# Performance work log

Hardware: AMD Instinct MI355X
Metric: run time of the kernel (lower is better)

Reference implementation:

```python
import jax, jax.numpy as jnp
import numpy as np

SUBSTEPS = 8  # fixed substeps per save interval (replaces diffrax adaptive PID control)

# Tsit5 (Tsitouras 2011) Butcher tableau, 5th-order solution weights
C2, C3, C4, C5, C6 = 0.161, 0.327, 0.9, 0.9800255409045097, 1.0
A21 = 0.161
A31, A32 = -0.008480655492356989, 0.335480655492357
A41, A42, A43 = 2.8971530571054935, -6.359448489975075, 4.3622954328695815
A51, A52, A53, A54 = 5.325864828439257, -11.748883564062828, 7.4955393428898365, -0.09249506636175525
A61, A62, A63, A64, A65 = 5.86145544294642, -12.92096931784711, 8.159367898576159, -0.071584973281401, -0.028269050394068383
B1, B2, B3, B4, B5, B6 = 0.09646076681806523, 0.01, 0.4798896504144996, 1.379008574103742, -3.290069515436081, 2.324710524099774

# SEIAR epidemiological constants (hardcoded in NODE.RHS)
KK, AA, II, P, F, EE, DD, Q = 0.526, 0.244, 0.244, 0.667, 0.98, 0.0, 1.0, 0.5


def setup_inputs() -> dict:
    key = jax.random.key(0)
    ks = jax.random.split(key, 4)
    W = 64  # width_size

    def lin(k, out_d, in_d):
        lim = 1.0 / np.sqrt(in_d)
        kw, kb = jax.random.split(k)
        w = jax.random.uniform(kw, (out_d, in_d), minval=-lim, maxval=lim, dtype=jnp.float32)
        b = jax.random.uniform(kb, (out_d,), minval=-lim, maxval=lim, dtype=jnp.float32)
        return w, b

    w_in, b_in = lin(ks[0], W, 1)   # MLP: 1 -> W
    w_h, b_h = lin(ks[1], W, W)     # W -> W (depth=2 => one hidden-to-hidden layer)
    w_out, b_out = lin(ks[2], 1, W) # W -> 1

    return {
        "y0_ignored": jax.random.normal(ks[3], (5,), dtype=jnp.float32),
        "ts": jnp.arange(1024, dtype=jnp.float32),
        "state_vec": jnp.array([5.0, -5.0, 0.0, -5.0, -5.0], dtype=jnp.float32),
        "w_in": w_in, "b_in": b_in,
        "w_h": w_h, "b_h": b_h,
        "w_out": w_out, "b_out": b_out,
        "scales": jnp.ones((5,), dtype=jnp.float32),
    }


def reference(y0_ignored, ts, state_vec, w_in, b_in, w_h, b_h, w_out, b_out, scales):
    def beta(t):
        h = jax.nn.softplus(w_in @ jnp.atleast_1d(t) + b_in)
        h = jax.nn.softplus(w_h @ h + b_h)
        o = w_out @ h + b_out
        return jax.nn.sigmoid(1e-4 * o)[0]

    def rhs(t, y):
        S, E, I, A, R = y * scales
        b = beta(t)
        LL = EE * E + (1.0 - Q) * I + DD * A
        dS = -b * S * LL
        dE = b * S * LL - KK * E
        dI = P * KK * E - AA * I
        dA = (1.0 - P) * KK * E - II * A
        dR = F * AA * I + II * A
        return jnp.stack([dS, dE, dI, dA, dR]) / scales

    def tsit5_step(t, y, h):
        k1 = rhs(t, y)
        k2 = rhs(t + C2 * h, y + h * A21 * k1)
        k3 = rhs(t + C3 * h, y + h * (A31 * k1 + A32 * k2))
        k4 = rhs(t + C4 * h, y + h * (A41 * k1 + A42 * k2 + A43 * k3))
        k5 = rhs(t + C5 * h, y + h * (A51 * k1 + A52 * k2 + A53 * k3 + A54 * k4))
        k6 = rhs(t + C6 * h, y + h * (A61 * k1 + A62 * k2 + A63 * k3 + A64 * k4 + A65 * k5))
        return y + h * (B1 * k1 + B2 * k2 + B3 * k3 + B4 * k4 + B5 * k5 + B6 * k6)

    y0 = jax.nn.softmax(state_vec) / scales  # learned initial condition, normalized

    def interval(y, tt):
        t0, t1 = tt
        h = (t1 - t0) / SUBSTEPS
        def body(yc, i):
            return tsit5_step(t0 + i.astype(yc.dtype) * h, yc, h), None
        y, _ = jax.lax.scan(body, y, jnp.arange(SUBSTEPS))
        return y, y

    _, ys = jax.lax.scan(interval, y0, (ts[:-1], ts[1:]))  # [T-1, 5]
    states_norm = jnp.concatenate([y0[None], ys], axis=0)  # [T, 5]
    return states_norm * scales
```

## Files before the change

kernel.cpp:

```cpp
#include <hip/hip_runtime.h>
#include <math.h>


#define NCHUNK 32
#define NTOTAL 1280
#define NPROD  (NTOTAL - NCHUNK)
#define TS     64
#define BURN_MAX_POLLS 16384

#define NI 1032
#define NH 1028
#define NI_ALLOC 1048
#define NH_ALLOC 1040
#define NCT 66

#define A21f 0.161f
#define A31f -0.008480655492356989f
#define A32f 0.335480655492357f
#define A41f 2.8971530571054935f
#define A42f -6.359448489975075f
#define A43f 4.3622954328695815f
#define A51f 5.325864828439257f
#define A52f -11.748883564062828f
#define A53f 7.4955393428898365f
#define A54f -0.09249506636175525f
#define A61f 5.86145544294642f
#define A62f -12.92096931784711f
#define A63f 8.159367898576159f
#define A64f -0.071584973281401f
#define A65f -0.028269050394068383f
#define B1f 0.09646076681806523f
#define B2f 0.01f
#define B3f 0.4798896504144996f
#define B4f 1.379008574103742f
#define B5f -3.290069515436081f
#define B6f 2.324710524099774f

typedef float v2f __attribute__((ext_vector_type(2)));
__device__ __forceinline__ v2f vfma(v2f a, v2f b, v2f c) {
    return __builtin_elementwise_fma(a, b, c);
}
__device__ __forceinline__ v2f splat2(float x) { return (v2f){x, x}; }

struct Bounds { int s[NCHUNK + 1]; };

__device__ const float g_cstage[6] = {
    0.0f, 0.161f, 0.327f, 0.9f, 0.9800255409045097f, 1.0f};

__device__ __forceinline__ float softplus_f(float x) {
    return fmaxf(x, 0.0f) + log1pf(expf(-fabsf(x)));
}
__device__ __forceinline__ int imin(int a, int b) { return a < b ? a : b; }

#define cKK  0.526f
#define cAA  0.244f
#define cII  0.244f
#define cPKK ((float)(0.667 * 0.526))
#define cQKK ((float)((1.0 - 0.667) * 0.526))
#define cFAA ((float)(0.98 * 0.244))

__device__ __forceinline__ void rhs2(v2f zSE, v2f zIA, float b,
                                     v2f& kSE, v2f& kIA, float& kR) {
    float S = zSE.x, E = zSE.y, I = zIA.x, A = zIA.y;
    float LL = fmaf(0.5f, I, A);
    float T  = (b * S) * LL;
    kSE = (v2f){-T, fmaf(-cKK, E, T)};
    kIA = (v2f){fmaf(cPKK, E, -cAA * I), fmaf(cQKK, E, -cII * A)};
    kR  = fmaf(cFAA, I, cII * A);
}

struct Tab2 {
    v2f a21,a31,a32,a41,a42,a43,a51,a52,a53,a54;
    v2f a61,a62,a63,a64,a65,b1,b2,b3,b4,b5,b6;
};
__device__ __forceinline__ Tab2 make_tab2(float h) {
    Tab2 t;
    t.a21=splat2(A21f*h); t.a31=splat2(A31f*h); t.a32=splat2(A32f*h);
    t.a41=splat2(A41f*h); t.a42=splat2(A42f*h); t.a43=splat2(A43f*h);
    t.a51=splat2(A51f*h); t.a52=splat2(A52f*h); t.a53=splat2(A53f*h);
    t.a54=splat2(A54f*h); t.a61=splat2(A61f*h); t.a62=splat2(A62f*h);
    t.a63=splat2(A63f*h); t.a64=splat2(A64f*h); t.a65=splat2(A65f*h);
    t.b1=splat2(B1f*h); t.b2=splat2(B2f*h); t.b3=splat2(B3f*h);
    t.b4=splat2(B4f*h); t.b5=splat2(B5f*h); t.b6=splat2(B6f*h);
    return t;
}

#define FOLD(dSE,dIA,dR, c, kSE,kIA,kR, pSE,pIA,pR) \
    dSE = vfma(T.c, kSE, pSE); dIA = vfma(T.c, kIA, pIA); \
    dR  = fmaf(T.c.x, kR, pR);

__device__ __forceinline__ void t5_step(v2f& zSE, v2f& zIA, float& zR,
                                        const Tab2& T, const float bc[6]) {
    v2f k1SE,k1IA,k2SE,k2IA,k3SE,k3IA,k4SE,k4IA,k5SE,k5IA,k6SE,k6IA;
    float k1R,k2R,k3R,k4R,k5R,k6R;
    v2f tSE,tIA,pSE,pIA; float tR,pR;

    rhs2(zSE,zIA,bc[0],k1SE,k1IA,k1R);
    FOLD(tSE,tIA,tR, a21, k1SE,k1IA,k1R, zSE,zIA,zR);
    rhs2(tSE,tIA,bc[1],k2SE,k2IA,k2R);
    FOLD(pSE,pIA,pR, a31, k1SE,k1IA,k1R, zSE,zIA,zR);
    FOLD(tSE,tIA,tR, a32, k2SE,k2IA,k2R, pSE,pIA,pR);
    rhs2(tSE,tIA,bc[2],k3SE,k3IA,k3R);
    FOLD(pSE,pIA,pR, a41, k1SE,k1IA,k1R, zSE,zIA,zR);
    FOLD(pSE,pIA,pR, a42, k2SE,k2IA,k2R, pSE,pIA,pR);
    FOLD(tSE,tIA,tR, a43, k3SE,k3IA,k3R, pSE,pIA,pR);
    rhs2(tSE,tIA,bc[3],k4SE,k4IA,k4R);
    FOLD(pSE,pIA,pR, a51, k1SE,k1IA,k1R, zSE,zIA,zR);
    FOLD(pSE,pIA,pR, a52, k2SE,k2IA,k2R, pSE,pIA,pR);
    FOLD(pSE,pIA,pR, a53, k3SE,k3IA,k3R, pSE,pIA,pR);
    FOLD(tSE,tIA,tR, a54, k4SE,k4IA,k4R, pSE,pIA,pR);
    rhs2(tSE,tIA,bc[4],k5SE,k5IA,k5R);
    FOLD(pSE,pIA,pR, a61, k1SE,k1IA,k1R, zSE,zIA,zR);
    FOLD(pSE,pIA,pR, a62, k2SE,k2IA,k2R, pSE,pIA,pR);
    FOLD(pSE,pIA,pR, a63, k3SE,k3IA,k3R, pSE,pIA,pR);
    FOLD(pSE,pIA,pR, a64, k4SE,k4IA,k4R, pSE,pIA,pR);
    FOLD(tSE,tIA,tR, a65, k5SE,k5IA,k5R, pSE,pIA,pR);
    rhs2(tSE,tIA,bc[5],k6SE,k6IA,k6R);
    FOLD(pSE,pIA,pR, b1, k1SE,k1IA,k1R, zSE,zIA,zR);
    FOLD(pSE,pIA,pR, b2, k2SE,k2IA,k2R, pSE,pIA,pR);
    FOLD(pSE,pIA,pR, b3, k3SE,k3IA,k3R, pSE,pIA,pR);
    FOLD(pSE,pIA,pR, b4, k4SE,k4IA,k4R, pSE,pIA,pR);
    FOLD(pSE,pIA,pR, b5, k5SE,k5IA,k5R, pSE,pIA,pR);
    FOLD(zSE,zIA,zR, b6, k6SE,k6IA,k6R, pSE,pIA,pR);
}

__device__ __forceinline__ void rk4_step(v2f& zSE, v2f& zIA, float& zR,
                                         v2f h2v, v2f hv, v2f h6v,
                                         float b0, float bm, float b1) {
    v2f k1SE,k1IA,k2SE,k2IA,k3SE,k3IA,k4SE,k4IA;
    float k1R,k2R,k3R,k4R;
    v2f tSE,tIA; float tR;
    const v2f two = splat2(2.0f);

    rhs2(zSE,zIA,b0,k1SE,k1IA,k1R);
    tSE=vfma(h2v,k1SE,zSE); tIA=vfma(h2v,k1IA,zIA); tR=fmaf(h2v.x,k1R,zR);
    rhs2(tSE,tIA,bm,k2SE,k2IA,k2R);
    tSE=vfma(h2v,k2SE,zSE); tIA=vfma(h2v,k2IA,zIA); tR=fmaf(h2v.x,k2R,zR);
    rhs2(tSE,tIA,bm,k3SE,k3IA,k3R);
    tSE=vfma(hv,k3SE,zSE);  tIA=vfma(hv,k3IA,zIA);  tR=fmaf(hv.x,k3R,zR);
    v2f PSE = vfma(two, k2SE + k3SE, k1SE);
    v2f PIA = vfma(two, k2IA + k3IA, k1IA);
    float PR = fmaf(2.0f, k2R + k3R, k1R);
    rhs2(tSE,tIA,b1,k4SE,k4IA,k4R);
    zSE = vfma(h6v, PSE + k4SE, zSE);
    zIA = vfma(h6v, PIA + k4IA, zIA);
    zR  = fmaf(h6v.x, PR + k4R, zR);
}

__device__ __forceinline__ float aload(const float* p) {
    return __hip_atomic_load(p, __ATOMIC_RELAXED, __HIP_MEMORY_SCOPE_AGENT);
}
__device__ __forceinline__ bool ok3(const float v[3]) {
    return (v[0] > 0.0f) && (v[1] > 0.0f) && (v[2] > 0.0f);
}
__device__ __forceinline__ bool ok6(const float v[6]) {
    return (v[0]>0.f)&&(v[1]>0.f)&&(v[2]>0.f)&&(v[3]>0.f)&&(v[4]>0.f)&&(v[5]>0.f);
}
__device__ __forceinline__ void loadF(float v[3], const float* bi,
                                      const float* bh, int i) {
    v[0] = aload(bi + i); v[1] = aload(bh + i); v[2] = aload(bi + i + 1);
}
__device__ __forceinline__ void loadC(float v[3], const float* bi, int j) {
    const float* p = bi + 256 + 4 * j;
    v[0] = aload(p); v[1] = aload(p + 2); v[2] = aload(p + 4);
}
__device__ __forceinline__ void load6(float v[6], const float* p) {
#pragma unroll
    for (int j = 0; j < 6; ++j) v[j] = aload(p + j);
}

__global__ __launch_bounds__(64, 1) void fused_kernel(
    const float* __restrict__ ts,
    const float* __restrict__ state_vec,
    const float* __restrict__ w_in, const float* __restrict__ b_in,
    const float* __restrict__ w_h,  const float* __restrict__ b_h,
    const float* __restrict__ w_out, const float* __restrict__ b_out,
    float* __restrict__ beta_int, float* __restrict__ beta_half,
    float* __restrict__ beta_cT,
    float* __restrict__ done_arr, float* __restrict__ out,
    Bounds B)
{
    int b    = blockIdx.x;
    int lane = threadIdx.x;

    if (b >= NCHUNK) {
        int p = b - NCHUNK;
        const int TtlPair = 2 * NH;
        const int Ttl = NCT * 6 + TtlPair + (NI - NH);
        float t0g = ts[0], hf = ts[1] - ts[0];
        float wi = w_in[lane], bi_ = b_in[lane];
        float bhh = b_h[lane], wo = w_out[lane];
        float bo = b_out[0];
        const float* __restrict__ wr = w_h + (lane << 6);

        for (int e = p; e < Ttl; e += NPROD) {
            float t; float* dst;
            if (e < NCT * 6) {
                int row = e / 6, st = e - row * 6;
                t = t0g + (4.0f * row + 4.0f * g_cstage[st]) * hf;
                dst = beta_cT + row * 8 + st;
            } else if (e < NCT * 6 + TtlPair) {
                int idx = e - NCT * 6;
                int i = idx >> 1;
                if (idx & 1) { t = t0g + ((float)i + 0.5f) * hf; dst = beta_half + i; }
                else         { t = t0g + (float)i * hf;          dst = beta_int + i;  }
            } else {
                int i = NH + (e - NCT * 6 - TtlPair);
                t = t0g + (float)i * hf; dst = beta_int + i;
            }
            float h1 = softplus_f(fmaf(wi, t, bi_));
            float acc = bhh;
#pragma unroll
            for (int k = 0; k < 64; ++k)
                acc = fmaf(wr[k], __shfl(h1, k, 64), acc);
            float h2 = softplus_f(acc);
            float pr = wo * h2;
#pragma unroll
            for (int off = 32; off > 0; off >>= 1)
                pr += __shfl_down(pr, off, 64);
            if (lane == 0) {
                float o  = pr + bo;
                float bb = 1.0f / (1.0f + expf(-1e-4f * o));
                __hip_atomic_store(dst, bb, __ATOMIC_RELAXED,
                                   __HIP_MEMORY_SCOPE_AGENT);
            }
        }

        float x[8];
#pragma unroll
        for (int j = 0; j < 8; ++j) x[j] = 1.0f + (float)(lane + j) * 1e-12f;
        for (int outer = 0; outer < BURN_MAX_POLLS; ++outer) {
            for (int i2 = 0; i2 < 40; ++i2) {
#pragma unroll
                for (int j = 0; j < 8; ++j)
                    x[j] = fmaf(x[j], 0.99999988f, 1e-9f);
            }
            float f = aload(done_arr + (lane & 31));
            if (__all(f == 1.0f)) break;
        }
        float r = 0.0f;
#pragma unroll
        for (int j = 0; j < 8; ++j) r += x[j];
        if (r == 123456.0f) done_arr[63] = r;
        return;
    }

    if (lane != 0) return;

    int start = B.s[b];
    int end   = B.s[b + 1];
    int nf    = end - start;
    float hf  = ts[1] - ts[0];

    v2f zSE, zIA; float zR;
    {
        float v[5], zz[5];
#pragma unroll
        for (int s = 0; s < 5; ++s) v[s] = state_vec[s];
        float m = v[0];
#pragma unroll
        for (int s = 1; s < 5; ++s) m = fmaxf(m, v[s]);
        float sum = 0.0f;
#pragma unroll
        for (int s = 0; s < 5; ++s) { zz[s] = expf(v[s] - m); sum += zz[s]; }
        float inv = 1.0f / sum;
#pragma unroll
        for (int s = 0; s < 5; ++s) zz[s] *= inv;
        zSE = (v2f){zz[0], zz[1]}; zIA = (v2f){zz[2], zz[3]}; zR = zz[4];
        if (b == 0) {
#pragma unroll
            for (int s = 0; s < 5; ++s) out[s] = zz[s];
        }
    }

    if (nf > 0) {
        int nc = start / 4;
        int nT = imin(nc, TS);
        int nR = nc - nT;

        if (nT > 0) {
            Tab2 T = make_tab2(4.0f * hf);
            float r0[6], r1[6], bc[6];
            load6(r0, beta_cT);
            load6(r1, beta_cT + 8);
            int i = 0;
            for (; i + 2 <= nT; i += 2) {
                const float* p0 = beta_cT + i * 8;
                while (!ok6(r0)) load6(r0, p0);
#pragma unroll
                for (int j = 0; j < 6; ++j) bc[j] = r0[j];
                load6(r0, p0 + 16);
                t5_step(zSE, zIA, zR, T, bc);
                const float* p1 = p0 + 8;
                while (!ok6(r1)) load6(r1, p1);
#pragma unroll
                for (int j = 0; j < 6; ++j) bc[j] = r1[j];
                load6(r1, p1 + 16);
                t5_step(zSE, zIA, zR, T, bc);
            }
            if (i < nT) {
                const float* p0 = beta_cT + i * 8;
                while (!ok6(r0)) load6(r0, p0);
#pragma unroll
                for (int j = 0; j < 6; ++j) bc[j] = r0[j];
                t5_step(zSE, zIA, zR, T, bc);
            }
        }

        if (nR > 0) {
            v2f h2v = splat2(2.0f * hf), hv = splat2(4.0f * hf),
                h6v = splat2(4.0f * hf / 6.0f);
            float r0[3], r1[3], r2[3], r3[3];
            loadC(r0, beta_int, 0); loadC(r1, beta_int, 1);
            loadC(r2, beta_int, 2); loadC(r3, beta_int, 3);
            int j = 0;
#define CSTEP(R, jj) { \
            while (!ok3(R)) loadC(R, beta_int, (jj)); \
            float b0_=R[0], bm_=R[1], b1_=R[2]; \
            loadC(R, beta_int, (jj) + 4); \
            rk4_step(zSE, zIA, zR, h2v, hv, h6v, b0_, bm_, b1_); }
            for (; j + 4 <= nR; j += 4) {
                CSTEP(r0, j) CSTEP(r1, j + 1) CSTEP(r2, j + 2) CSTEP(r3, j + 3)
            }
            if (j < nR) { while(!ok3(r0)) loadC(r0,beta_int,j);
                rk4_step(zSE,zIA,zR,h2v,hv,h6v,r0[0],r0[1],r0[2]); j++; }
            if (j < nR) { while(!ok3(r1)) loadC(r1,beta_int,j);
                rk4_step(zSE,zIA,zR,h2v,hv,h6v,r1[0],r1[1],r1[2]); j++; }
            if (j < nR) { while(!ok3(r2)) loadC(r2,beta_int,j);
                rk4_step(zSE,zIA,zR,h2v,hv,h6v,r2[0],r2[1],r2[2]); j++; }
#undef CSTEP
        }

        {
            v2f h2v = splat2(0.5f * hf), hv = splat2(hf),
                h6v = splat2(hf / 6.0f);
            float r0[3], r1[3], r2[3], r3[3];
            loadF(r0, beta_int, beta_half, start);
            loadF(r1, beta_int, beta_half, start + 1);
            loadF(r2, beta_int, beta_half, start + 2);
            loadF(r3, beta_int, beta_half, start + 3);
            int i = 0;
#define FSTEP(R, ii) { \
            int gi = start + (ii); \
            while (!ok3(R)) loadF(R, beta_int, beta_half, gi); \
            float b0_=R[0], bm_=R[1], b1_=R[2]; \
            loadF(R, beta_int, beta_half, gi + 4); \
            rk4_step(zSE, zIA, zR, h2v, hv, h6v, b0_, bm_, b1_); \
            float* op = out + (size_t)(gi + 1) * 5; \
            op[0]=zSE.x; op[1]=zSE.y; op[2]=zIA.x; op[3]=zIA.y; op[4]=zR; }
            for (; i + 4 <= nf; i += 4) {
                FSTEP(r0, i) FSTEP(r1, i + 1) FSTEP(r2, i + 2) FSTEP(r3, i + 3)
            }
#define FTAIL(R) { \
            int gi = start + i; \
            while (!ok3(R)) loadF(R, beta_int, beta_half, gi); \
            rk4_step(zSE, zIA, zR, h2v, hv, h6v, R[0], R[1], R[2]); \
            float* op = out + (size_t)(gi + 1) * 5; \
            op[0]=zSE.x; op[1]=zSE.y; op[2]=zIA.x; op[3]=zIA.y; op[4]=zR; i++; }
            if (i < nf) FTAIL(r0)
            if (i < nf) FTAIL(r1)
            if (i < nf) FTAIL(r2)
#undef FSTEP
#undef FTAIL
        }
    }

    __hip_atomic_store(done_arr + b, 1.0f, __ATOMIC_RELAXED,
                       __HIP_MEMORY_SCOPE_AGENT);
}

extern "C" void kernel_launch(void* const* d_in, const int* in_sizes, int n_in,
                              void* d_out, int out_size, void* d_ws, size_t ws_size,
                              hipStream_t stream)
{
    const float* ts        = (const float*)d_in[1];
    const float* state_vec = (const float*)d_in[2];
    const float* w_in      = (const float*)d_in[3];
    const float* b_in      = (const float*)d_in[4];
    const float* w_h       = (const float*)d_in[5];
    const float* b_h       = (const float*)d_in[6];
    const float* w_out     = (const float*)d_in[7];
    const float* b_out     = (const float*)d_in[8];
    float* out = (float*)d_out;

    int n_t   = in_sizes[1];
    int n_int = n_t - 1;

    auto costR = [](float s) {
        float a = s < 256.f ? s : 256.f;
        float c = s > 256.f ? s - 256.f : 0.f;
        return 0.25f * a + 0.15f * c;
    };
    auto cover = [&](float D) {
        float s = 0.f;
        for (int bb = 0; bb < NCHUNK; ++bb) {
            float f = (D - costR(s)) / 0.6f;
            int fi = ((int)(f / 4.f)) * 4;
            if (fi < 4) fi = 4;
            s += (float)fi;
        }
        return (int)s;
    };
    float lo = 4.f, hi = 1200.f;
    for (int it = 0; it < 48; ++it) {
        float mid = 0.5f * (lo + hi);
        if (cover(mid) >= n_int) hi = mid; else lo = mid;
    }
    float D = hi;
    Bounds B;
    {
        float s = 0.f; B.s[0] = 0;
        for (int bb = 0; bb < NCHUNK; ++bb) {
            float f = (D - costR(s)) / 0.6f;
            int fi = ((int)(f / 4.f)) * 4;
            if (fi < 4) fi = 4;
            s += (float)fi;
            int si = (int)s;
            if (si > n_int) si = n_int;
            B.s[bb + 1] = si;
            s = (float)si;
        }
        B.s[NCHUNK] = n_int;
    }

    float* beta_int  = (float*)d_ws;
    float* beta_half = beta_int + NI_ALLOC;
    float* beta_cT   = beta_half + NH_ALLOC;
    float* done_arr  = beta_cT + (size_t)68 * 8;

    fused_kernel<<<NTOTAL, 64, 0, stream>>>(
        ts, state_vec, w_in, b_in, w_h, b_h, w_out, b_out,
        beta_int, beta_half, beta_cT, done_arr, out, B);
}
```

Measured before the change: 130.8 us.

## Replace per-value polling with global producer barrier and packed float4 beta rows

```diff
diff --git a/kernel.cpp b/kernel.cpp
--- a/kernel.cpp
+++ b/kernel.cpp
@@ -8,11 +8,14 @@
 #define TS     64
 #define BURN_MAX_POLLS 16384
 
-#define NI 1032
-#define NH 1028
-#define NI_ALLOC 1048
-#define NH_ALLOC 1040
-#define NCT 66
+#define NT5R   66
+#define NBI    1024
+#define NBH    1023
+#define TTOTAL (NT5R * 6 + NBI + NBH)
+
+#define ROWT_ALLOC 68
+#define ROWC_ALLOC 200
+#define ROWF_ALLOC 1032
 
 #define A21f 0.161f
 #define A31f -0.008480655492356989f
@@ -147,37 +150,15 @@
     zR  = fmaf(h6v.x, PR + k4R, zR);
 }
 
-__device__ __forceinline__ float aload(const float* p) {
-    return __hip_atomic_load(p, __ATOMIC_RELAXED, __HIP_MEMORY_SCOPE_AGENT);
-}
-__device__ __forceinline__ bool ok3(const float v[3]) {
-    return (v[0] > 0.0f) && (v[1] > 0.0f) && (v[2] > 0.0f);
-}
-__device__ __forceinline__ bool ok6(const float v[6]) {
-    return (v[0]>0.f)&&(v[1]>0.f)&&(v[2]>0.f)&&(v[3]>0.f)&&(v[4]>0.f)&&(v[5]>0.f);
-}
-__device__ __forceinline__ void loadF(float v[3], const float* bi,
-                                      const float* bh, int i) {
-    v[0] = aload(bi + i); v[1] = aload(bh + i); v[2] = aload(bi + i + 1);
-}
-__device__ __forceinline__ void loadC(float v[3], const float* bi, int j) {
-    const float* p = bi + 256 + 4 * j;
-    v[0] = aload(p); v[1] = aload(p + 2); v[2] = aload(p + 4);
-}
-__device__ __forceinline__ void load6(float v[6], const float* p) {
-#pragma unroll
-    for (int j = 0; j < 6; ++j) v[j] = aload(p + j);
-}
-
 __global__ __launch_bounds__(64, 1) void fused_kernel(
     const float* __restrict__ ts,
     const float* __restrict__ state_vec,
     const float* __restrict__ w_in, const float* __restrict__ b_in,
     const float* __restrict__ w_h,  const float* __restrict__ b_h,
     const float* __restrict__ w_out, const float* __restrict__ b_out,
-    float* __restrict__ beta_int, float* __restrict__ beta_half,
-    float* __restrict__ beta_cT,
-    float* __restrict__ done_arr, float* __restrict__ out,
+    unsigned int* __restrict__ prod_done, float* __restrict__ done_arr,
+    float* __restrict__ rowT, float4* __restrict__ rowC,
+    float4* __restrict__ rowF, float* __restrict__ out,
     Bounds B)
 {
     int b    = blockIdx.x;
@@ -185,28 +166,25 @@
 
     if (b >= NCHUNK) {
         int p = b - NCHUNK;
-        const int TtlPair = 2 * NH;
-        const int Ttl = NCT * 6 + TtlPair + (NI - NH);
         float t0g = ts[0], hf = ts[1] - ts[0];
         float wi = w_in[lane], bi_ = b_in[lane];
         float bhh = b_h[lane], wo = w_out[lane];
         float bo = b_out[0];
         const float* __restrict__ wr = w_h + (lane << 6);
-
-        for (int e = p; e < Ttl; e += NPROD) {
-            float t; float* dst;
-            if (e < NCT * 6) {
+        float* rowCf = (float*)rowC;
+        float* rowFf = (float*)rowF;
+
+        for (int e = p; e < TTOTAL; e += NPROD) {
+            float t;
+            if (e < NT5R * 6) {
                 int row = e / 6, st = e - row * 6;
                 t = t0g + (4.0f * row + 4.0f * g_cstage[st]) * hf;
-                dst = beta_cT + row * 8 + st;
-            } else if (e < NCT * 6 + TtlPair) {
-                int idx = e - NCT * 6;
-                int i = idx >> 1;
-                if (idx & 1) { t = t0g + ((float)i + 0.5f) * hf; dst = beta_half + i; }
-                else         { t = t0g + (float)i * hf;          dst = beta_int + i;  }
+            } else if (e < NT5R * 6 + NBI) {
+                int i = e - NT5R * 6;
+                t = t0g + (float)i * hf;
             } else {
-                int i = NH + (e - NCT * 6 - TtlPair);
-                t = t0g + (float)i * hf; dst = beta_int + i;
+                int i = e - NT5R * 6 - NBI;
+                t = t0g + ((float)i + 0.5f) * hf;
             }
             float h1 = softplus_f(fmaf(wi, t, bi_));
             float acc = bhh;
@@ -221,10 +199,31 @@
             if (lane == 0) {
                 float o  = pr + bo;
                 float bb = 1.0f / (1.0f + expf(-1e-4f * o));
-                __hip_atomic_store(dst, bb, __ATOMIC_RELAXED,
+                if (e < NT5R * 6) {
+                    rowT[(e / 6) * 8 + (e % 6)] = bb;
+                } else if (e < NT5R * 6 + NBI) {
+                    int i = e - NT5R * 6;
+                    if (i < 1023) rowFf[i * 4 + 0] = bb;
+                    if (i >= 1)   rowFf[(i - 1) * 4 + 2] = bb;
+                    if (i >= 256 && (i & 1) == 0) {
+                        int d = i - 256;
+                        int j = d >> 2;
+                        if ((d & 3) == 0) {
+                            if (j < ROWC_ALLOC) rowCf[j * 4 + 0] = bb;
+                            if (j >= 1)         rowCf[(j - 1) * 4 + 2] = bb;
+                        } else {
+                            if (j < ROWC_ALLOC) rowCf[j * 4 + 1] = bb;
+                        }
+                    }
+                } else {
+                    int i = e - NT5R * 6 - NBI;
+                    rowFf[i * 4 + 1] = bb;
+                }
+            }
+        }
+        if (lane == 0)
+            __hip_atomic_fetch_add(prod_done, 1u, __ATOMIC_RELEASE,
                                    __HIP_MEMORY_SCOPE_AGENT);
-            }
-        }
 
         float x[8];
 #pragma unroll
@@ -235,7 +234,9 @@
                 for (int j = 0; j < 8; ++j)
                     x[j] = fmaf(x[j], 0.99999988f, 1e-9f);
             }
-            float f = aload(done_arr + (lane & 31));
+            float f = __hip_atomic_load(done_arr + (lane & 31),
+                                        __ATOMIC_RELAXED,
+                                        __HIP_MEMORY_SCOPE_AGENT);
             if (__all(f == 1.0f)) break;
         }
         float r = 0.0f;
@@ -273,6 +274,11 @@
         }
     }
 
+    while (__hip_atomic_load(prod_done, __ATOMIC_RELAXED,
+                             __HIP_MEMORY_SCOPE_AGENT) < NPROD) {}
+    (void)__hip_atomic_load(prod_done, __ATOMIC_ACQUIRE,
+                            __HIP_MEMORY_SCOPE_AGENT);
+
     if (nf > 0) {
         int nc = start / 4;
         int nT = imin(nc, TS);
@@ -280,29 +286,23 @@
 
         if (nT > 0) {
             Tab2 T = make_tab2(4.0f * hf);
-            float r0[6], r1[6], bc[6];
-            load6(r0, beta_cT);
-            load6(r1, beta_cT + 8);
+            float4 q0 = *(const float4*)(rowT);
+            float2 s0 = *(const float2*)(rowT + 4);
+            float4 q1 = *(const float4*)(rowT + 8);
+            float2 s1 = *(const float2*)(rowT + 12);
             int i = 0;
             for (; i + 2 <= nT; i += 2) {
-                const float* p0 = beta_cT + i * 8;
-                while (!ok6(r0)) load6(r0, p0);
-#pragma unroll
-                for (int j = 0; j < 6; ++j) bc[j] = r0[j];
-                load6(r0, p0 + 16);
+                float bc[6] = {q0.x,q0.y,q0.z,q0.w,s0.x,s0.y};
+                q0 = *(const float4*)(rowT + (i + 2) * 8);
+                s0 = *(const float2*)(rowT + (i + 2) * 8 + 4);
                 t5_step(zSE, zIA, zR, T, bc);
-                const float* p1 = p0 + 8;
-                while (!ok6(r1)) load6(r1, p1);
-#pragma unroll
-                for (int j = 0; j < 6; ++j) bc[j] = r1[j];
-                load6(r1, p1 + 16);
-                t5_step(zSE, zIA, zR, T, bc);
+                float bd[6] = {q1.x,q1.y,q1.z,q1.w,s1.x,s1.y};
+                q1 = *(const float4*)(rowT + (i + 3) * 8);
+                s1 = *(const float2*)(rowT + (i + 3) * 8 + 4);
+                t5_step(zSE, zIA, zR, T, bd);
             }
             if (i < nT) {
-                const float* p0 = beta_cT + i * 8;
-                while (!ok6(r0)) load6(r0, p0);
-#pragma unroll
-                for (int j = 0; j < 6; ++j) bc[j] = r0[j];
+                float bc[6] = {q0.x,q0.y,q0.z,q0.w,s0.x,s0.y};
                 t5_step(zSE, zIA, zR, T, bc);
             }
         }
@@ -310,58 +310,51 @@
         if (nR > 0) {
             v2f h2v = splat2(2.0f * hf), hv = splat2(4.0f * hf),
                 h6v = splat2(4.0f * hf / 6.0f);
-            float r0[3], r1[3], r2[3], r3[3];
-            loadC(r0, beta_int, 0); loadC(r1, beta_int, 1);
-            loadC(r2, beta_int, 2); loadC(r3, beta_int, 3);
+            float4 c0 = rowC[0], c1 = rowC[1], c2 = rowC[2], c3 = rowC[3];
             int j = 0;
-#define CSTEP(R, jj) { \
-            while (!ok3(R)) loadC(R, beta_int, (jj)); \
-            float b0_=R[0], bm_=R[1], b1_=R[2]; \
-            loadC(R, beta_int, (jj) + 4); \
-            rk4_step(zSE, zIA, zR, h2v, hv, h6v, b0_, bm_, b1_); }
             for (; j + 4 <= nR; j += 4) {
-                CSTEP(r0, j) CSTEP(r1, j + 1) CSTEP(r2, j + 2) CSTEP(r3, j + 3)
-            }
-            if (j < nR) { while(!ok3(r0)) loadC(r0,beta_int,j);
-                rk4_step(zSE,zIA,zR,h2v,hv,h6v,r0[0],r0[1],r0[2]); j++; }
-            if (j < nR) { while(!ok3(r1)) loadC(r1,beta_int,j);
-                rk4_step(zSE,zIA,zR,h2v,hv,h6v,r1[0],r1[1],r1[2]); j++; }
-            if (j < nR) { while(!ok3(r2)) loadC(r2,beta_int,j);
-                rk4_step(zSE,zIA,zR,h2v,hv,h6v,r2[0],r2[1],r2[2]); j++; }
-#undef CSTEP
+                float4 u;
+                u = c0; c0 = rowC[j + 4];
+                rk4_step(zSE,zIA,zR,h2v,hv,h6v,u.x,u.y,u.z);
+                u = c1; c1 = rowC[j + 5];
+                rk4_step(zSE,zIA,zR,h2v,hv,h6v,u.x,u.y,u.z);
+                u = c2; c2 = rowC[j + 6];
+                rk4_step(zSE,zIA,zR,h2v,hv,h6v,u.x,u.y,u.z);
+                u = c3; c3 = rowC[j + 7];
+                rk4_step(zSE,zIA,zR,h2v,hv,h6v,u.x,u.y,u.z);
+            }
+            if (j < nR) { rk4_step(zSE,zIA,zR,h2v,hv,h6v,c0.x,c0.y,c0.z); j++; }
+            if (j < nR) { rk4_step(zSE,zIA,zR,h2v,hv,h6v,c1.x,c1.y,c1.z); j++; }
+            if (j < nR) { rk4_step(zSE,zIA,zR,h2v,hv,h6v,c2.x,c2.y,c2.z); j++; }
         }
 
         {
             v2f h2v = splat2(0.5f * hf), hv = splat2(hf),
-                h6v = splat2(hf / 6.0f);
-            float r0[3], r1[3], r2[3], r3[3];
-            loadF(r0, beta_int, beta_half, start);
-            loadF(r1, beta_int, beta_half, start + 1);
-            loadF(r2, beta_int, beta_half, start + 2);
-            loadF(r3, beta_int, beta_half, start + 3);
+                h6v = splat2(hf * (1.0f / 6.0f));
+            const float4* RF = rowF + start;
+            float4 r0 = RF[0], r1 = RF[1], r2 = RF[2], r3 = RF[3];
             int i = 0;
-#define FSTEP(R, ii) { \
-            int gi = start + (ii); \
-            while (!ok3(R)) loadF(R, beta_int, beta_half, gi); \
-            float b0_=R[0], bm_=R[1], b1_=R[2]; \
-            loadF(R, beta_int, beta_half, gi + 4); \
-            rk4_step(zSE, zIA, zR, h2v, hv, h6v, b0_, bm_, b1_); \
-            float* op = out + (size_t)(gi + 1) * 5; \
+#define FSTORE(ii) { \
+            float* op = out + (size_t)(start + (ii) + 1) * 5; \
             op[0]=zSE.x; op[1]=zSE.y; op[2]=zIA.x; op[3]=zIA.y; op[4]=zR; }
             for (; i + 4 <= nf; i += 4) {
-                FSTEP(r0, i) FSTEP(r1, i + 1) FSTEP(r2, i + 2) FSTEP(r3, i + 3)
-            }
-#define FTAIL(R) { \
-            int gi = start + i; \
-            while (!ok3(R)) loadF(R, beta_int, beta_half, gi); \
-            rk4_step(zSE, zIA, zR, h2v, hv, h6v, R[0], R[1], R[2]); \
-            float* op = out + (size_t)(gi + 1) * 5; \
-            op[0]=zSE.x; op[1]=zSE.y; op[2]=zIA.x; op[3]=zIA.y; op[4]=zR; i++; }
-            if (i < nf) FTAIL(r0)
-            if (i < nf) FTAIL(r1)
-            if (i < nf) FTAIL(r2)
-#undef FSTEP
-#undef FTAIL
+                float4 u;
+                u = r0; r0 = RF[i + 4];
+                rk4_step(zSE,zIA,zR,h2v,hv,h6v,u.x,u.y,u.z); FSTORE(i)
+                u = r1; r1 = RF[i + 5];
+                rk4_step(zSE,zIA,zR,h2v,hv,h6v,u.x,u.y,u.z); FSTORE(i + 1)
+                u = r2; r2 = RF[i + 6];
+                rk4_step(zSE,zIA,zR,h2v,hv,h6v,u.x,u.y,u.z); FSTORE(i + 2)
+                u = r3; r3 = RF[i + 7];
+                rk4_step(zSE,zIA,zR,h2v,hv,h6v,u.x,u.y,u.z); FSTORE(i + 3)
+            }
+            if (i < nf) { rk4_step(zSE,zIA,zR,h2v,hv,h6v,r0.x,r0.y,r0.z);
+                          FSTORE(i) i++; }
+            if (i < nf) { rk4_step(zSE,zIA,zR,h2v,hv,h6v,r1.x,r1.y,r1.z);
+                          FSTORE(i) i++; }
+            if (i < nf) { rk4_step(zSE,zIA,zR,h2v,hv,h6v,r2.x,r2.y,r2.z);
+                          FSTORE(i) i++; }
+#undef FSTORE
         }
     }
 
@@ -423,12 +416,16 @@
         B.s[NCHUNK] = n_int;
     }
 
-    float* beta_int  = (float*)d_ws;
-    float* beta_half = beta_int + NI_ALLOC;
-    float* beta_cT   = beta_half + NH_ALLOC;
-    float* done_arr  = beta_cT + (size_t)68 * 8;
+    float* ctrl  = (float*)d_ws;
+    unsigned int* prod_done = (unsigned int*)ctrl;
+    float* done_arr = ctrl + 4;
+    float* rowT  = ctrl + 68;
+    float4* rowC = (float4*)(rowT + (size_t)ROWT_ALLOC * 8);
+    float4* rowF = rowC + ROWC_ALLOC;
+
+    hipMemsetAsync(ctrl, 0, 68 * sizeof(float), stream);
 
     fused_kernel<<<NTOTAL, 64, 0, stream>>>(
         ts, state_vec, w_in, b_in, w_h, b_h, w_out, b_out,
-        beta_int, beta_half, beta_cT, done_arr, out, B);
-}
+        prod_done, done_arr, rowT, rowC, rowF, out, B);
+}
```

After: 198.4 us. +51.7%, slower.
